# Performance work log

Measured on AMD Instinct MI355X. Metric: run time of the kernel, lower is better.

Reference implementation:

```python
import jax, jax.numpy as jnp
import numpy as np

D_MODEL = 1024
NUM_HEADS = 16
DEPTH = D_MODEL // NUM_HEADS
LN_EPS = 1e-5


def setup_inputs() -> dict:
    key = jax.random.key(0)
    ks = jax.random.split(key, 12)
    B, S, D = 4, 2048, D_MODEL
    s = 1.0 / np.sqrt(D)
    inp = {
        "Q": jax.random.normal(ks[0], (B, S, D), jnp.float32),
        "K": jax.random.normal(ks[1], (B, S, D), jnp.float32),
        "V": jax.random.normal(ks[2], (B, S, D), jnp.float32),
        "mask": jnp.ones((B, 1, 1, S), jnp.int32),
        "Wq": jax.random.normal(ks[3], (D, D), jnp.float32) * s,
        "bq": jnp.zeros((D,), jnp.float32),
        "Wk": jax.random.normal(ks[4], (D, D), jnp.float32) * s,
        "bk": jnp.zeros((D,), jnp.float32),
        "Wv": jax.random.normal(ks[5], (D, D), jnp.float32) * s,
        "bv": jnp.zeros((D,), jnp.float32),
        "Wo": jax.random.normal(ks[6], (D, D), jnp.float32) * s,
        "bo": jnp.zeros((D,), jnp.float32),
        "gamma": jnp.ones((D,), jnp.float32),
        "beta": jnp.zeros((D,), jnp.float32),
    }
    return inp


def _split_heads(x, B, S):
    # (B, S, D) -> (B, H, S, depth)
    return x.reshape(B, S, NUM_HEADS, DEPTH).transpose(0, 2, 1, 3)


def reference(Q, K, V, mask, Wq, bq, Wk, bk, Wv, bv, Wo, bo, gamma, beta):
    B, S, D = Q.shape
    q = _split_heads(Q @ Wq.T + bq, B, S)  # (B,H,S,dh)
    k = _split_heads(K @ Wk.T + bk, B, S)
    v = _split_heads(V @ Wv.T + bv, B, S)
    scores = jnp.einsum('bhqd,bhkd->bhqk', q, k) / jnp.sqrt(jnp.asarray(DEPTH, q.dtype))
    scores = jnp.where(mask == 0, jnp.asarray(-1e9, scores.dtype), scores)
    attn = jax.nn.softmax(scores, axis=-1)
    ctx = jnp.einsum('bhqk,bhkd->bhqd', attn, v)            # (B,H,S,dh)
    ctx = ctx.transpose(0, 2, 1, 3).reshape(B, S, D)        # merge heads
    out = ctx @ Wo.T + bo
    # residual with the input Q + LayerNorm
    x = out + Q
    mu = jnp.mean(x, axis=-1, keepdims=True)
    var = jnp.mean(jnp.square(x - mu), axis=-1, keepdims=True)
    return gamma * (x - mu) * jax.lax.rsqrt(var + LN_EPS) + beta
```

## Files before the change

kernel.cpp:

```cpp
#include <hip/hip_runtime.h>

#define SEQ 2048
#define BB 4
#define DM 1024
#define NH 16
#define DH 64
#define ROWS (BB*SEQ)

#define BM 128
#define BN 128
#define BK 32
#define KSTEPS (DM / BK)

#define KVBLK 32
#define NT (SEQ / KVBLK)
#define NBUF 3

typedef _Float16 f16;
typedef _Float16 f16x8 __attribute__((ext_vector_type(8)));
typedef _Float16 f16x4 __attribute__((ext_vector_type(4)));
typedef float f32x4 __attribute__((ext_vector_type(4)));
typedef float f32x16 __attribute__((ext_vector_type(16)));
typedef unsigned u32x4 __attribute__((ext_vector_type(4)));

__device__ __forceinline__ f32x4 mfma16(f16x8 a, f16x8 b, f32x4 c) {
    return __builtin_amdgcn_mfma_f32_16x16x32_f16(a, b, c, 0, 0, 0);
}
__device__ __forceinline__ f32x16 mfma32(f16x8 a, f16x8 b, f32x16 c) {
    return __builtin_amdgcn_mfma_f32_32x32x16_f16(a, b, c, 0, 0, 0);
}
__device__ __forceinline__ unsigned pkh(float a, float b) {
    auto h = __builtin_amdgcn_cvt_pkrtz(a, b);
    return __builtin_bit_cast(unsigned, h);
}
__device__ __forceinline__ void plswap(unsigned& a, unsigned& b) {
    auto r = __builtin_amdgcn_permlane32_swap((int)a, (int)b, false, false);
    a = (unsigned)r[0];
    b = (unsigned)r[1];
}
__device__ __forceinline__ float2 plswapf(float x) {
    int xi = __builtin_bit_cast(int, x);
    auto r = __builtin_amdgcn_permlane32_swap(xi, xi, false, false);
    return float2{ __builtin_bit_cast(float, (int)r[0]), __builtin_bit_cast(float, (int)r[1]) };
}
typedef const __attribute__((address_space(1))) void gvoid;
typedef __attribute__((address_space(3))) void lvoid;
__device__ __forceinline__ void gload16(const f16* g, f16* l) {
    __builtin_amdgcn_global_load_lds((gvoid*)g, (lvoid*)l, 16, 0, 0);
}

__global__ __launch_bounds__(256) void cvt_weights(
    const float* __restrict__ wq, const float* __restrict__ wk,
    const float* __restrict__ wv, const float* __restrict__ wo,
    f16* __restrict__ oq, f16* __restrict__ ok,
    f16* __restrict__ ov, f16* __restrict__ oo,
    const int* __restrict__ mask, unsigned* __restrict__ pm) {
    if (blockIdx.x == 0) {
        int tid = threadIdx.x;
        const int* mp = mask + (size_t)tid * 32;
        unsigned bits = 0;
#pragma unroll
        for (int j = 0; j < 32; ++j) bits |= (mp[j] != 0 ? 1u : 0u) << j;
        pm[tid] = bits;
    }
    int i = (blockIdx.x * 256 + threadIdx.x) * 4;
    float4 a = *(const float4*)(wq + i);
    float4 b = *(const float4*)(wk + i);
    float4 c = *(const float4*)(wv + i);
    float4 d = *(const float4*)(wo + i);
    f16x4 va = { (f16)a.x, (f16)a.y, (f16)a.z, (f16)a.w };
    f16x4 vb = { (f16)b.x, (f16)b.y, (f16)b.z, (f16)b.w };
    f16x4 vc = { (f16)c.x, (f16)c.y, (f16)c.z, (f16)c.w };
    f16x4 vd = { (f16)d.x, (f16)d.y, (f16)d.z, (f16)d.w };
    *(f16x4*)(oq + i) = va;
    *(f16x4*)(ok + i) = vb;
    *(f16x4*)(ov + i) = vc;
    *(f16x4*)(oo + i) = vd;
}

__global__ __launch_bounds__(256) void gemm_proj3(
    const float* __restrict__ Qf, const float* __restrict__ Kf,
    const float* __restrict__ Vf,
    const f16* __restrict__ wq, const f16* __restrict__ wk,
    const f16* __restrict__ wv,
    const float* __restrict__ bq, const float* __restrict__ bk,
    const float* __restrict__ bv,
    f16* __restrict__ q16o, f16* __restrict__ k16o, f16* __restrict__ v16o,
    float qscale) {
    const float* A; const f16* W; const float* bias; f16* out;
    float scale; int mode;
    if (blockIdx.z == 0)      { A = Qf; W = wq; bias = bq; out = q16o; scale = qscale; mode = 0; }
    else if (blockIdx.z == 1) { A = Kf; W = wk; bias = bk; out = k16o; scale = 1.0f;   mode = 0; }
    else                      { A = Vf; W = wv; bias = bv; out = v16o; scale = 1.0f;   mode = 2; }

    __shared__ f16 lds_a[2][BM][BK + 8];
    __shared__ f16 lds_b[2][BN][BK];
    const int tid = threadIdx.x;
    const int lane = tid & 63;
    const int wv_ = tid >> 6;
    const int wr = wv_ >> 1, wc = wv_ & 1;
    const int lo = lane & 15, hi = lane >> 4;
    const int rowbase = blockIdx.x * BM;
    const int colbase = blockIdx.y * BN;
    const int ar = tid >> 1;
    const int ac = (tid & 1) * 16;

    f32x4 acc[4][4];
#pragma unroll
    for (int m = 0; m < 4; ++m)
#pragma unroll
        for (int n = 0; n < 4; ++n) acc[m][n] = (f32x4){0.f, 0.f, 0.f, 0.f};

    float4 av0, av1, av2, av3;
#define LOAD_A(k0)                                                                  \
    {                                                                               \
        const float* ap_ = A + (size_t)(rowbase + ar) * DM + (k0) + ac;             \
        av0 = *(const float4*)(ap_);                                                \
        av1 = *(const float4*)(ap_ + 4);                                            \
        av2 = *(const float4*)(ap_ + 8);                                            \
        av3 = *(const float4*)(ap_ + 12);                                           \
    }
#define WRITE_A(buf)                                                                \
    {                                                                               \
        f16* dp_ = &lds_a[buf][ar][ac];                                             \
        u32x4 t0_ = { pkh(av0.x, av0.y), pkh(av0.z, av0.w),                         \
                      pkh(av1.x, av1.y), pkh(av1.z, av1.w) };                       \
        u32x4 t1_ = { pkh(av2.x, av2.y), pkh(av2.z, av2.w),                         \
                      pkh(av3.x, av3.y), pkh(av3.z, av3.w) };                       \
        *(u32x4*)(dp_) = t0_;                                                       \
        *(u32x4*)(dp_ + 8) = t1_;                                                   \
    }
#define STAGE_W(buf, k0)                                                            \
    {                                                                               \
        int r_ = lane >> 2, kc_ = (lane & 3) * 8;                                   \
        gload16(W + (size_t)(colbase + wv_ * 16 + r_) * DM + (k0) + kc_,            \
                &lds_b[buf][wv_ * 16][0]);                                          \
        gload16(W + (size_t)(colbase + (wv_ + 4) * 16 + r_) * DM + (k0) + kc_,      \
                &lds_b[buf][(wv_ + 4) * 16][0]);                                    \
    }

    LOAD_A(0)
    STAGE_W(0, 0)
    WRITE_A(0)
    __syncthreads();
    int buf = 0;
    for (int ks = 0; ks < KSTEPS; ++ks) {
        if (ks + 1 < KSTEPS) {
            LOAD_A((ks + 1) * BK)
            STAGE_W(buf ^ 1, (ks + 1) * BK)
        }
        f16x8 af[4], bf[4];
#pragma unroll
        for (int m = 0; m < 4; ++m)
            af[m] = *(const f16x8*)&lds_a[buf][wr * 64 + m * 16 + lo][hi * 8];
#pragma unroll
        for (int n = 0; n < 4; ++n)
            bf[n] = *(const f16x8*)&lds_b[buf][wc * 64 + n * 16 + lo][hi * 8];
#pragma unroll
        for (int m = 0; m < 4; ++m)
#pragma unroll
            for (int n = 0; n < 4; ++n)
                acc[m][n] = mfma16(af[m], bf[n], acc[m][n]);
        if (ks + 1 < KSTEPS) WRITE_A(buf ^ 1)
        __syncthreads();
        buf ^= 1;
    }
#undef LOAD_A
#undef WRITE_A
#undef STAGE_W

#pragma unroll
    for (int n = 0; n < 4; ++n) {
        int col = colbase + wc * 64 + n * 16 + lo;
        float bv_ = bias[col];
        int hh = col >> 6, dh = col & 63;
#pragma unroll
        for (int m = 0; m < 4; ++m)
#pragma unroll
            for (int r = 0; r < 4; ++r) {
                int row = rowbase + wr * 64 + m * 16 + hi * 4 + r;
                int bi = row >> 11;
                int ss = row & (SEQ - 1);
                float v = (acc[m][n][r] + bv_) * scale;
                size_t dst;
                if (mode == 2)
                    dst = (((size_t)(bi * NH + hh) * DH + dh) * SEQ + ss);
                else
                    dst = (((size_t)(bi * NH + hh) * SEQ + ss) * DH + dh);
                out[dst] = (f16)v;
            }
    }
}

__global__ __launch_bounds__(256) void gemm_oproj(
    const f16* __restrict__ A, const f16* __restrict__ W,
    const float* __restrict__ bo, const float* __restrict__ Qin,
    float* __restrict__ out) {
    __shared__ f16 lds_a[2][BM][BK];
    __shared__ f16 lds_b[2][BN][BK];
    const int lane = threadIdx.x & 63;
    const int wv = threadIdx.x >> 6;
    const int wr = wv >> 1, wc = wv & 1;
    const int lo = lane & 15, hi = lane >> 4;
    const int rowbase = blockIdx.x * BM;
    const int colbase = blockIdx.y * BN;

    f32x4 acc[4][4];
#pragma unroll
    for (int m = 0; m < 4; ++m)
#pragma unroll
        for (int n = 0; n < 4; ++n) acc[m][n] = (f32x4){0.f, 0.f, 0.f, 0.f};

#define STAGE_TILES(buf, k0)                                                        \
    {                                                                               \
        int r_ = lane >> 2, kc_ = (lane & 3) * 8;                                   \
        gload16(A + (size_t)(rowbase + wv * 16 + r_) * DM + (k0) + kc_,             \
                &lds_a[buf][wv * 16][0]);                                           \
        gload16(A + (size_t)(rowbase + (wv + 4) * 16 + r_) * DM + (k0) + kc_,       \
                &lds_a[buf][(wv + 4) * 16][0]);                                     \
        gload16(W + (size_t)(colbase + wv * 16 + r_) * DM + (k0) + kc_,             \
                &lds_b[buf][wv * 16][0]);                                           \
        gload16(W + (size_t)(colbase + (wv + 4) * 16 + r_) * DM + (k0) + kc_,       \
                &lds_b[buf][(wv + 4) * 16][0]);                                     \
    }

    STAGE_TILES(0, 0)
    __syncthreads();
    int buf = 0;
    for (int ks = 0; ks < KSTEPS; ++ks) {
        if (ks + 1 < KSTEPS) STAGE_TILES(buf ^ 1, (ks + 1) * BK)
        f16x8 af[4], bf[4];
#pragma unroll
        for (int m = 0; m < 4; ++m)
            af[m] = *(const f16x8*)&lds_a[buf][wr * 64 + m * 16 + lo][hi * 8];
#pragma unroll
        for (int n = 0; n < 4; ++n)
            bf[n] = *(const f16x8*)&lds_b[buf][wc * 64 + n * 16 + lo][hi * 8];
#pragma unroll
        for (int m = 0; m < 4; ++m)
#pragma unroll
            for (int n = 0; n < 4; ++n)
                acc[m][n] = mfma16(af[m], bf[n], acc[m][n]);
        __syncthreads();
        buf ^= 1;
    }
#undef STAGE_TILES

#pragma unroll
    for (int n = 0; n < 4; ++n) {
        int col = colbase + wc * 64 + n * 16 + lo;
        float bv = bo[col];
#pragma unroll
        for (int m = 0; m < 4; ++m)
#pragma unroll
            for (int r = 0; r < 4; ++r) {
                int row = rowbase + wr * 64 + m * 16 + hi * 4 + r;
                size_t idx = (size_t)row * DM + col;
                out[idx] = acc[m][n][r] + bv + Qin[idx];
            }
    }
}

__global__ __launch_bounds__(256, 3) void attn_kernel(
    const f16* __restrict__ q16, const f16* __restrict__ k16,
    const f16* __restrict__ v16t, const unsigned* __restrict__ pm,
    f16* __restrict__ out16) {
    __shared__ f16 smem[NBUF][2][KVBLK * 64];
    const int tid = threadIdx.x;
    const int lane = tid & 63;
    const int wv = tid >> 6;
    const int lo = lane & 31, hw = lane >> 5;
    const int bh = blockIdx.y;
    const int b = bh >> 4, hd = bh & 15;
    const int q0 = blockIdx.x * 128 + wv * 32;

    const f16* qp = q16 + ((size_t)bh * SEQ + q0 + lo) * DH + hw * 8;
    const f16* kp = k16 + (size_t)bh * SEQ * DH;
    const f16* vp = v16t + (size_t)bh * DH * SEQ;
    const unsigned* pmb = pm + b * 64;

    const int sr = lane >> 3, scb = lane & 7;
    const int cb = scb ^ sr;
    const int svr = lane >> 2, svc = lane & 3;
    const int cbv = svc ^ (svr & 3);

    f16x8 qb[4];
#pragma unroll
    for (int c = 0; c < 4; ++c) qb[c] = *(const f16x8*)(qp + c * 16);

    f32x16 fz;
#pragma unroll
    for (int i = 0; i < 16; ++i) fz[i] = 0.f;
    f32x16 ctx0 = fz, ctx1 = fz;
    float l = 0.f;

#define STAGE(buf, KB)                                                              \
    {                                                                               \
        gload16(kp + (size_t)((KB) + wv * 8 + sr) * DH + cb * 8,                    \
                &smem[buf][0][wv * 512]);                                           \
        gload16(vp + (size_t)(wv * 16 + svr) * SEQ + (KB) + cbv * 8,                \
                &smem[buf][1][wv * 512]);                                           \
    }

    STAGE(0, 0)
    STAGE(1, KVBLK)

    int bc = 0;
    for (int t = 0; t < NT; ++t) {
        if (t < NT - 1) asm volatile("s_waitcnt vmcnt(2)" ::: "memory");
        else            asm volatile("s_waitcnt vmcnt(0)" ::: "memory");
        __builtin_amdgcn_s_barrier();
        asm volatile("" ::: "memory");

        const f16* kbase = &smem[bc][0][0];
        const f16* vbase = &smem[bc][1][0];

        f16x8 kf0 = *(const f16x8*)&kbase[lo * 64 + (((0 + hw) ^ (lo & 7)) << 3)];
        f16x8 kf1 = *(const f16x8*)&kbase[lo * 64 + (((2 + hw) ^ (lo & 7)) << 3)];

        if (t + 2 < NT) {
            int bs = bc + 2; if (bs >= NBUF) bs -= NBUF;
            STAGE(bs, (t + 2) * KVBLK)
        }

        f32x16 st;
        __builtin_amdgcn_s_setprio(1);
        st = mfma32(kf0, qb[0], fz);
        f16x8 kf2 = *(const f16x8*)&kbase[lo * 64 + (((4 + hw) ^ (lo & 7)) << 3)];
        st = mfma32(kf1, qb[1], st);
        f16x8 kf3 = *(const f16x8*)&kbase[lo * 64 + (((6 + hw) ^ (lo & 7)) << 3)];
        st = mfma32(kf2, qb[2], st);
        st = mfma32(kf3, qb[3], st);
        __builtin_amdgcn_s_setprio(0);

        unsigned bm = pmb[t];
        if (bm != 0xffffffffu) {
            unsigned bs_ = bm >> (hw * 4);
#pragma unroll
            for (int r = 0; r < 16; ++r)
                if (!((bs_ >> ((r & 3) + 8 * (r >> 2))) & 1)) st[r] = -1e9f;
        }

        float ts = 0.f;
#pragma unroll
        for (int i = 0; i < 16; ++i) { st[i] = exp2f(st[i]); ts += st[i]; }
        {
            float2 pp = plswapf(ts);
            ts = pp.x + pp.y;
        }
        l += ts;

        __builtin_amdgcn_s_setprio(1);
        {
            unsigned w0 = pkh(st[0], st[1]),   w1 = pkh(st[2], st[3]);
            unsigned w2 = pkh(st[4], st[5]),   w3 = pkh(st[6], st[7]);
            unsigned w4 = pkh(st[8], st[9]),   w5 = pkh(st[10], st[11]);
            unsigned w6 = pkh(st[12], st[13]), w7 = pkh(st[14], st[15]);
            f16x8 vf00 = *(const f16x8*)&vbase[(0 * 32 + lo) * 32 + (((0 + hw) ^ (lo & 3)) << 3)];
            f16x8 vf10 = *(const f16x8*)&vbase[(1 * 32 + lo) * 32 + (((0 + hw) ^ (lo & 3)) << 3)];
            {
                unsigned a0 = w0, b0 = w2; plswap(a0, b0);
                unsigned a1 = w1, b1 = w3; plswap(a1, b1);
                u32x4 t_ = { a0, a1, b0, b1 };
                f16x8 pb = __builtin_bit_cast(f16x8, t_);
                ctx0 = mfma32(vf00, pb, ctx0);
                ctx1 = mfma32(vf10, pb, ctx1);
            }
            f16x8 vf01 = *(const f16x8*)&vbase[(0 * 32 + lo) * 32 + (((2 + hw) ^ (lo & 3)) << 3)];
            f16x8 vf11 = *(const f16x8*)&vbase[(1 * 32 + lo) * 32 + (((2 + hw) ^ (lo & 3)) << 3)];
            {
                unsigned a0 = w4, b0 = w6; plswap(a0, b0);
                unsigned a1 = w5, b1 = w7; plswap(a1, b1);
                u32x4 t_ = { a0, a1, b0, b1 };
                f16x8 pb = __builtin_bit_cast(f16x8, t_);
                ctx0 = mfma32(vf01, pb, ctx0);
                ctx1 = mfma32(vf11, pb, ctx1);
            }
        }
        __builtin_amdgcn_s_setprio(0);

        bc = (bc + 1 == NBUF) ? 0 : bc + 1;
    }
#undef STAGE

    __syncthreads();

    float rl = 1.0f / l;
    f16* tbp = &smem[0][0][0] + wv * (32 * 66);
#pragma unroll
    for (int u = 0; u < 8; ++u) {
        int d0 = 2 * (u & 1) + 8 * (u >> 1) + 4 * hw;
        unsigned pw0 = pkh(ctx0[2 * u] * rl, ctx0[2 * u + 1] * rl);
        unsigned pw1 = pkh(ctx1[2 * u] * rl, ctx1[2 * u + 1] * rl);
        *(unsigned*)&tbp[lo * 66 + d0] = pw0;
        *(unsigned*)&tbp[lo * 66 + 32 + d0] = pw1;
    }
    __syncthreads();
#pragma unroll
    for (int it = 0; it < 4; ++it) {
        int r = it * 8 + (lane >> 3);
        const unsigned* src = (const unsigned*)(tbp + r * 66);
        int cc = (lane & 7) * 4;
        u32x4 t = { src[cc], src[cc + 1], src[cc + 2], src[cc + 3] };
        f16x8 vvv = __builtin_bit_cast(f16x8, t);
        *(f16x8*)(out16 + ((size_t)(b * SEQ) + q0 + r) * DM + hd * 64 + (lane & 7) * 8) = vvv;
    }
}

__global__ __launch_bounds__(256) void ln_kernel(
    float* __restrict__ x, const float* __restrict__ gamma,
    const float* __restrict__ beta) {
    const int lane = threadIdx.x & 63;
    const int wave = threadIdx.x >> 6;
    const int row = blockIdx.x * 4 + wave;
    float* rp = x + (size_t)row * DM;

    float4 v[4];
#pragma unroll
    for (int j = 0; j < 4; ++j) v[j] = ((const float4*)rp)[lane + 64 * j];

    float sum = 0.f;
#pragma unroll
    for (int j = 0; j < 4; ++j) sum += v[j].x + v[j].y + v[j].z + v[j].w;
#pragma unroll
    for (int off = 1; off < 64; off <<= 1) sum += __shfl_xor(sum, off);
    float mean = sum * (1.f / DM);

    float vs = 0.f;
#pragma unroll
    for (int j = 0; j < 4; ++j) {
        float dx = v[j].x - mean, dy = v[j].y - mean, dz = v[j].z - mean, dw = v[j].w - mean;
        vs += dx * dx + dy * dy + dz * dz + dw * dw;
    }
#pragma unroll
    for (int off = 1; off < 64; off <<= 1) vs += __shfl_xor(vs, off);
    float rstd = rsqrtf(vs * (1.f / DM) + 1e-5f);

#pragma unroll
    for (int j = 0; j < 4; ++j) {
        int idx = lane + 64 * j;
        float4 g = ((const float4*)gamma)[idx];
        float4 bt = ((const float4*)beta)[idx];
        float4 o;
        o.x = (v[j].x - mean) * rstd * g.x + bt.x;
        o.y = (v[j].y - mean) * rstd * g.y + bt.y;
        o.z = (v[j].z - mean) * rstd * g.z + bt.z;
        o.w = (v[j].w - mean) * rstd * g.w + bt.w;
        ((float4*)rp)[idx] = o;
    }
}

extern "C" void kernel_launch(void* const* d_in, const int* in_sizes, int n_in,
                              void* d_out, int out_size, void* d_ws, size_t ws_size,
                              hipStream_t stream) {
    const float* Q    = (const float*)d_in[0];
    const float* K    = (const float*)d_in[1];
    const float* V    = (const float*)d_in[2];
    const int*   mask = (const int*)d_in[3];
    const float* Wq   = (const float*)d_in[4];
    const float* bq   = (const float*)d_in[5];
    const float* Wk   = (const float*)d_in[6];
    const float* bk   = (const float*)d_in[7];
    const float* Wv   = (const float*)d_in[8];
    const float* bv   = (const float*)d_in[9];
    const float* Wo   = (const float*)d_in[10];
    const float* bo   = (const float*)d_in[11];
    const float* gamma = (const float*)d_in[12];
    const float* beta  = (const float*)d_in[13];
    float* out = (float*)d_out;

    char* ws = (char*)d_ws;
    const size_t MB = 1024 * 1024;
    f16* wq16 = (f16*)(ws + 0 * MB);
    f16* wk16 = (f16*)(ws + 2 * MB);
    f16* wv16 = (f16*)(ws + 4 * MB);
    f16* wo16 = (f16*)(ws + 6 * MB);
    f16* c16  = (f16*)(ws + 8 * MB);
    f16* q16  = (f16*)(ws + 24 * MB);
    f16* k16  = (f16*)(ws + 40 * MB);
    f16* v16t = (f16*)(ws + 56 * MB);

    unsigned* pm = (unsigned*)((char*)d_out + (size_t)out_size * 4 - 4096);

    cvt_weights<<<dim3(DM * DM / (256 * 4)), dim3(256), 0, stream>>>(
        Wq, Wk, Wv, Wo, wq16, wk16, wv16, wo16, mask, pm);

    const float qscale = 0.125f * 1.44269504f;

    gemm_proj3<<<dim3(ROWS / BM, DM / BN, 3), dim3(256), 0, stream>>>(
        Q, K, V, wq16, wk16, wv16, bq, bk, bv, q16, k16, v16t, qscale);

    attn_kernel<<<dim3(SEQ / 128, BB * NH), dim3(256), 0, stream>>>(
        q16, k16, v16t, pm, c16);

    gemm_oproj<<<dim3(ROWS / BM, DM / BN), dim3(256), 0, stream>>>(
        c16, wo16, bo, Q, out);

    ln_kernel<<<dim3(ROWS / 4), dim3(256), 0, stream>>>(out, gamma, beta);
}
```

Measured before the change: 270.9 us.

## Switch LDS tiles to k-chunk-major layout and split fused QKV launch

Shared-memory tiles in the projection GEMMs, the output GEMM and the attention K/V staging change from row-major with XOR swizzle to a layout where each 8-element k-chunk is contiguous across rows. Global async loads now fetch one row per lane, and the fragment reads drop the swizzle arithmetic. The fused three-way projection kernel is also split back into three separate launches. This aims to avoid LDS bank conflicts and simplify indexing, but per-lane row-strided global loads may coalesce worse, and the extra launches remove the cross-projection concurrency the fused grid had.

```diff
diff --git a/kernel.cpp b/kernel.cpp
--- a/kernel.cpp
+++ b/kernel.cpp
@@ -78,27 +78,16 @@
     *(f16x4*)(oo + i) = vd;
 }
 
-__global__ __launch_bounds__(256) void gemm_proj3(
-    const float* __restrict__ Qf, const float* __restrict__ Kf,
-    const float* __restrict__ Vf,
-    const f16* __restrict__ wq, const f16* __restrict__ wk,
-    const f16* __restrict__ wv,
-    const float* __restrict__ bq, const float* __restrict__ bk,
-    const float* __restrict__ bv,
-    f16* __restrict__ q16o, f16* __restrict__ k16o, f16* __restrict__ v16o,
-    float qscale) {
-    const float* A; const f16* W; const float* bias; f16* out;
-    float scale; int mode;
-    if (blockIdx.z == 0)      { A = Qf; W = wq; bias = bq; out = q16o; scale = qscale; mode = 0; }
-    else if (blockIdx.z == 1) { A = Kf; W = wk; bias = bk; out = k16o; scale = 1.0f;   mode = 0; }
-    else                      { A = Vf; W = wv; bias = bv; out = v16o; scale = 1.0f;   mode = 2; }
-
+__global__ __launch_bounds__(256) void gemm_proj(
+    const float* __restrict__ A, const f16* __restrict__ W,
+    const float* __restrict__ bias, f16* __restrict__ out,
+    float scale, int mode) {
     __shared__ f16 lds_a[2][BM][BK + 8];
-    __shared__ f16 lds_b[2][BN][BK];
+    __shared__ f16 lds_b[2][BN * BK];
     const int tid = threadIdx.x;
     const int lane = tid & 63;
-    const int wv_ = tid >> 6;
-    const int wr = wv_ >> 1, wc = wv_ & 1;
+    const int wv = tid >> 6;
+    const int wr = wv >> 1, wc = wv & 1;
     const int lo = lane & 15, hi = lane >> 4;
     const int rowbase = blockIdx.x * BM;
     const int colbase = blockIdx.y * BN;
@@ -132,11 +121,12 @@
     }
 #define STAGE_W(buf, k0)                                                            \
     {                                                                               \
-        int r_ = lane >> 2, kc_ = (lane & 3) * 8;                                   \
-        gload16(W + (size_t)(colbase + wv_ * 16 + r_) * DM + (k0) + kc_,            \
-                &lds_b[buf][wv_ * 16][0]);                                          \
-        gload16(W + (size_t)(colbase + (wv_ + 4) * 16 + r_) * DM + (k0) + kc_,      \
-                &lds_b[buf][(wv_ + 4) * 16][0]);                                    \
+        gload16(W + (size_t)(colbase + (wv & 1) * 64 + lane) * DM + (k0)            \
+                    + (wv >> 1) * 8,                                                \
+                &lds_b[buf][wv * 512]);                                             \
+        gload16(W + (size_t)(colbase + ((wv + 4) & 1) * 64 + lane) * DM + (k0)      \
+                    + ((wv + 4) >> 1) * 8,                                          \
+                &lds_b[buf][(wv + 4) * 512]);                                       \
     }
 
     LOAD_A(0)
@@ -155,7 +145,7 @@
             af[m] = *(const f16x8*)&lds_a[buf][wr * 64 + m * 16 + lo][hi * 8];
 #pragma unroll
         for (int n = 0; n < 4; ++n)
-            bf[n] = *(const f16x8*)&lds_b[buf][wc * 64 + n * 16 + lo][hi * 8];
+            bf[n] = *(const f16x8*)&lds_b[buf][hi * 1024 + (wc * 64 + n * 16 + lo) * 8];
 #pragma unroll
         for (int m = 0; m < 4; ++m)
 #pragma unroll
@@ -196,8 +186,8 @@
     const f16* __restrict__ A, const f16* __restrict__ W,
     const float* __restrict__ bo, const float* __restrict__ Qin,
     float* __restrict__ out) {
-    __shared__ f16 lds_a[2][BM][BK];
-    __shared__ f16 lds_b[2][BN][BK];
+    __shared__ f16 lds_a[2][BM * BK];
+    __shared__ f16 lds_b[2][BN * BK];
     const int lane = threadIdx.x & 63;
     const int wv = threadIdx.x >> 6;
     const int wr = wv >> 1, wc = wv & 1;
@@ -213,15 +203,18 @@
 
 #define STAGE_TILES(buf, k0)                                                        \
     {                                                                               \
-        int r_ = lane >> 2, kc_ = (lane & 3) * 8;                                   \
-        gload16(A + (size_t)(rowbase + wv * 16 + r_) * DM + (k0) + kc_,             \
-                &lds_a[buf][wv * 16][0]);                                           \
-        gload16(A + (size_t)(rowbase + (wv + 4) * 16 + r_) * DM + (k0) + kc_,       \
-                &lds_a[buf][(wv + 4) * 16][0]);                                     \
-        gload16(W + (size_t)(colbase + wv * 16 + r_) * DM + (k0) + kc_,             \
-                &lds_b[buf][wv * 16][0]);                                           \
-        gload16(W + (size_t)(colbase + (wv + 4) * 16 + r_) * DM + (k0) + kc_,       \
-                &lds_b[buf][(wv + 4) * 16][0]);                                     \
+        gload16(A + (size_t)(rowbase + (wv & 1) * 64 + lane) * DM + (k0)            \
+                    + (wv >> 1) * 8,                                                \
+                &lds_a[buf][wv * 512]);                                             \
+        gload16(A + (size_t)(rowbase + ((wv + 4) & 1) * 64 + lane) * DM + (k0)      \
+                    + ((wv + 4) >> 1) * 8,                                          \
+                &lds_a[buf][(wv + 4) * 512]);                                       \
+        gload16(W + (size_t)(colbase + (wv & 1) * 64 + lane) * DM + (k0)            \
+                    + (wv >> 1) * 8,                                                \
+                &lds_b[buf][wv * 512]);                                             \
+        gload16(W + (size_t)(colbase + ((wv + 4) & 1) * 64 + lane) * DM + (k0)      \
+                    + ((wv + 4) >> 1) * 8,                                          \
+                &lds_b[buf][(wv + 4) * 512]);                                       \
     }
 
     STAGE_TILES(0, 0)
@@ -232,10 +225,10 @@
         f16x8 af[4], bf[4];
 #pragma unroll
         for (int m = 0; m < 4; ++m)
-            af[m] = *(const f16x8*)&lds_a[buf][wr * 64 + m * 16 + lo][hi * 8];
+            af[m] = *(const f16x8*)&lds_a[buf][hi * 1024 + (wr * 64 + m * 16 + lo) * 8];
 #pragma unroll
         for (int n = 0; n < 4; ++n)
-            bf[n] = *(const f16x8*)&lds_b[buf][wc * 64 + n * 16 + lo][hi * 8];
+            bf[n] = *(const f16x8*)&lds_b[buf][hi * 1024 + (wc * 64 + n * 16 + lo) * 8];
 #pragma unroll
         for (int m = 0; m < 4; ++m)
 #pragma unroll
@@ -279,11 +272,6 @@
     const f16* vp = v16t + (size_t)bh * DH * SEQ;
     const unsigned* pmb = pm + b * 64;
 
-    const int sr = lane >> 3, scb = lane & 7;
-    const int cb = scb ^ sr;
-    const int svr = lane >> 2, svc = lane & 3;
-    const int cbv = svc ^ (svr & 3);
-
     f16x8 qb[4];
 #pragma unroll
     for (int c = 0; c < 4; ++c) qb[c] = *(const f16x8*)(qp + c * 16);
@@ -296,9 +284,9 @@
 
 #define STAGE(buf, KB)                                                              \
     {                                                                               \
-        gload16(kp + (size_t)((KB) + wv * 8 + sr) * DH + cb * 8,                    \
+        gload16(kp + (size_t)((KB) + (lane & 31)) * DH + (2 * wv + (lane >> 5)) * 8,\
                 &smem[buf][0][wv * 512]);                                           \
-        gload16(vp + (size_t)(wv * 16 + svr) * SEQ + (KB) + cbv * 8,                \
+        gload16(vp + (size_t)lane * SEQ + (KB) + wv * 8,                            \
                 &smem[buf][1][wv * 512]);                                           \
     }
 
@@ -315,8 +303,8 @@
         const f16* kbase = &smem[bc][0][0];
         const f16* vbase = &smem[bc][1][0];
 
-        f16x8 kf0 = *(const f16x8*)&kbase[lo * 64 + (((0 + hw) ^ (lo & 7)) << 3)];
-        f16x8 kf1 = *(const f16x8*)&kbase[lo * 64 + (((2 + hw) ^ (lo & 7)) << 3)];
+        f16x8 kf0 = *(const f16x8*)&kbase[(0 + hw) * 256 + lo * 8];
+        f16x8 kf1 = *(const f16x8*)&kbase[(2 + hw) * 256 + lo * 8];
 
         if (t + 2 < NT) {
             int bs = bc + 2; if (bs >= NBUF) bs -= NBUF;
@@ -326,9 +314,9 @@
         f32x16 st;
         __builtin_amdgcn_s_setprio(1);
         st = mfma32(kf0, qb[0], fz);
-        f16x8 kf2 = *(const f16x8*)&kbase[lo * 64 + (((4 + hw) ^ (lo & 7)) << 3)];
+        f16x8 kf2 = *(const f16x8*)&kbase[(4 + hw) * 256 + lo * 8];
         st = mfma32(kf1, qb[1], st);
-        f16x8 kf3 = *(const f16x8*)&kbase[lo * 64 + (((6 + hw) ^ (lo & 7)) << 3)];
+        f16x8 kf3 = *(const f16x8*)&kbase[(6 + hw) * 256 + lo * 8];
         st = mfma32(kf2, qb[2], st);
         st = mfma32(kf3, qb[3], st);
         __builtin_amdgcn_s_setprio(0);
@@ -356,8 +344,8 @@
             unsigned w2 = pkh(st[4], st[5]),   w3 = pkh(st[6], st[7]);
             unsigned w4 = pkh(st[8], st[9]),   w5 = pkh(st[10], st[11]);
             unsigned w6 = pkh(st[12], st[13]), w7 = pkh(st[14], st[15]);
-            f16x8 vf00 = *(const f16x8*)&vbase[(0 * 32 + lo) * 32 + (((0 + hw) ^ (lo & 3)) << 3)];
-            f16x8 vf10 = *(const f16x8*)&vbase[(1 * 32 + lo) * 32 + (((0 + hw) ^ (lo & 3)) << 3)];
+            f16x8 vf00 = *(const f16x8*)&vbase[(0 + hw) * 512 + (0 * 32 + lo) * 8];
+            f16x8 vf10 = *(const f16x8*)&vbase[(0 + hw) * 512 + (1 * 32 + lo) * 8];
             {
                 unsigned a0 = w0, b0 = w2; plswap(a0, b0);
                 unsigned a1 = w1, b1 = w3; plswap(a1, b1);
@@ -366,8 +354,8 @@
                 ctx0 = mfma32(vf00, pb, ctx0);
                 ctx1 = mfma32(vf10, pb, ctx1);
             }
-            f16x8 vf01 = *(const f16x8*)&vbase[(0 * 32 + lo) * 32 + (((2 + hw) ^ (lo & 3)) << 3)];
-            f16x8 vf11 = *(const f16x8*)&vbase[(1 * 32 + lo) * 32 + (((2 + hw) ^ (lo & 3)) << 3)];
+            f16x8 vf01 = *(const f16x8*)&vbase[(2 + hw) * 512 + (0 * 32 + lo) * 8];
+            f16x8 vf11 = *(const f16x8*)&vbase[(2 + hw) * 512 + (1 * 32 + lo) * 8];
             {
                 unsigned a0 = w4, b0 = w6; plswap(a0, b0);
                 unsigned a1 = w5, b1 = w7; plswap(a1, b1);
@@ -485,16 +473,17 @@
     cvt_weights<<<dim3(DM * DM / (256 * 4)), dim3(256), 0, stream>>>(
         Wq, Wk, Wv, Wo, wq16, wk16, wv16, wo16, mask, pm);
 
+    const dim3 ggrid(ROWS / BM, DM / BN);
     const float qscale = 0.125f * 1.44269504f;
 
-    gemm_proj3<<<dim3(ROWS / BM, DM / BN, 3), dim3(256), 0, stream>>>(
-        Q, K, V, wq16, wk16, wv16, bq, bk, bv, q16, k16, v16t, qscale);
+    gemm_proj<<<ggrid, dim3(256), 0, stream>>>(Q, wq16, bq, q16, qscale, 0);
+    gemm_proj<<<ggrid, dim3(256), 0, stream>>>(K, wk16, bk, k16, 1.0f, 0);
+    gemm_proj<<<ggrid, dim3(256), 0, stream>>>(V, wv16, bv, v16t, 1.0f, 2);
 
     attn_kernel<<<dim3(SEQ / 128, BB * NH), dim3(256), 0, stream>>>(
         q16, k16, v16t, pm, c16);
 
-    gemm_oproj<<<dim3(ROWS / BM, DM / BN), dim3(256), 0, stream>>>(
-        c16, wo16, bo, Q, out);
+    gemm_oproj<<<ggrid, dim3(256), 0, stream>>>(c16, wo16, bo, Q, out);
 
     ln_kernel<<<dim3(ROWS / 4), dim3(256), 0, stream>>>(out, gamma, beta);
 }
```

New measurement: 304.2 us. 1.12x slower.
